# Kernel tuning notes

Hardware: AMD Instinct MI355X
Metric: run time of the kernel (lower is better)

Reference implementation:

```python
import jax, jax.numpy as jnp
import numpy as np

N = 500000
H = 256
HET = 3
AH = 128
B = 64


def setup_inputs() -> dict:
    key = jax.random.key(0)
    ks = jax.random.split(key, 6)
    x = jax.random.normal(ks[0], (N, H), dtype=jnp.float32)
    het = jax.random.uniform(ks[1], (N, HET), dtype=jnp.float32)
    batch = jnp.sort(jax.random.randint(ks[2], (N,), 0, B)).astype(jnp.int64)
    # xavier-uniform linear weights (stored already transposed: [in, out])
    def xavier(k, fan_in, fan_out):
        bound = np.sqrt(6.0 / (fan_in + fan_out))
        return jax.random.uniform(k, (fan_in, fan_out), dtype=jnp.float32,
                                  minval=-bound, maxval=bound)
    W1 = xavier(ks[3], H + HET, AH)
    b1 = jnp.zeros((AH,), dtype=jnp.float32)
    W2 = xavier(ks[4], AH, 1)
    b2 = jnp.zeros((1,), dtype=jnp.float32)
    Wv = xavier(ks[5], H, H)
    bv = jnp.zeros((H,), dtype=jnp.float32)
    return {"x": x, "het": het, "batch": batch,
            "W1": W1, "b1": b1, "W2": W2, "b2": b2, "Wv": Wv, "bv": bv}


def reference(x, het, batch, W1, b1, W2, b2, Wv, bv):
    # gate MLP: Linear -> tanh -> Linear, on [h_i ; het_i]
    gate_in = jnp.concatenate([x, het], axis=-1)              # [N, H+HET]
    raw = jnp.tanh(gate_in @ W1 + b1) @ W2 + b2               # [N, 1]
    # per-graph (segment) softmax over nodes
    seg_max = jax.ops.segment_max(raw, batch, num_segments=B)  # [B, 1]
    seg_max = jnp.where(jnp.isfinite(seg_max), seg_max, 0.0)   # empty segments
    e = jnp.exp(raw - seg_max[batch])                          # [N, 1]
    denom = jax.ops.segment_sum(e, batch, num_segments=B)      # [B, 1]
    attn = e / denom[batch]                                    # [N, 1]
    # weighted scatter-sum of projected values
    values = x @ Wv + bv                                       # [N, H]
    z = jax.ops.segment_sum(attn * values, batch, num_segments=B)  # [B, H]
    return z, attn
```

## Files before the change

kernel.cpp:

```cpp
#include <hip/hip_runtime.h>
#include <hip/hip_fp16.h>

#define H 256
#define HETD 3
#define AH 128
#define BSEG 64

typedef _Float16 half8 __attribute__((ext_vector_type(8)));
typedef __attribute__((ext_vector_type(4))) float f32x4;

__global__ void pack_w1_kernel(const float* __restrict__ W1,
                               unsigned short* __restrict__ W1p) {
    int idx = blockIdx.x * 256 + threadIdx.x;
    if (idx >= 9 * 8 * 64 * 8) return;
    int j    = idx & 7;
    int lane = (idx >> 3) & 63;
    int nt   = (idx >> 9) & 7;
    int t    = idx >> 12;
    int n = nt * 16 + (lane & 15);
    int k = t * 32 + ((lane >> 4) & 3) * 8 + j;
    float w = (k < (H + HETD)) ? W1[k * AH + n] : 0.f;
    __half hw = __float2half(w);
    W1p[idx] = __half_as_ushort(hw);
}

__device__ __forceinline__ _Float16 f2h(float f) { return (_Float16)f; }

__global__ __launch_bounds__(256) void gate_kernel(
    const float* __restrict__ x, const float* __restrict__ het,
    const int* __restrict__ batch, const unsigned short* __restrict__ W1p,
    const float* __restrict__ b1, const float* __restrict__ W2,
    const float* __restrict__ b2, float* __restrict__ p,
    float* __restrict__ d, int n_nodes)
{
    __shared__ float sW2[AH];
    __shared__ float sb1[AH];
    __shared__ float sd[BSEG];
    int tid = threadIdx.x;
    if (tid < AH) { sW2[tid] = W2[tid]; sb1[tid] = b1[tid]; }
    if (tid < BSEG) sd[tid] = 0.f;
    __syncthreads();

    int lane = tid & 63;
    int wv   = tid >> 6;
    int row  = lane & 15;
    int quad = lane >> 4;
    long long base = ((long long)blockIdx.x * 4 + wv) * 64;

    if (base < n_nodes) {
        f32x4 acc[4][8] = {};
        int nodeA[4];
#pragma unroll
        for (int m = 0; m < 4; ++m) {
            long long nd = base + m * 16 + row;
            nodeA[m] = (int)(nd < n_nodes ? nd : (long long)(n_nodes - 1));
        }
        const uint4* W1p4 = (const uint4*)W1p;

        for (int t = 0; t < 8; ++t) {
            half8 a[4];
#pragma unroll
            for (int m = 0; m < 4; ++m) {
                const float4* xr =
                    (const float4*)(x + (size_t)nodeA[m] * H + t * 32 + quad * 8);
                float4 lo = xr[0];
                float4 hi = xr[1];
                half8 av;
                av[0] = f2h(lo.x); av[1] = f2h(lo.y);
                av[2] = f2h(lo.z); av[3] = f2h(lo.w);
                av[4] = f2h(hi.x); av[5] = f2h(hi.y);
                av[6] = f2h(hi.z); av[7] = f2h(hi.w);
                a[m] = av;
            }
#pragma unroll
            for (int nt = 0; nt < 8; ++nt) {
                union { uint4 u; half8 h; } cv;
                cv.u = W1p4[(t * 8 + nt) * 64 + lane];
#pragma unroll
                for (int m = 0; m < 4; ++m)
                    acc[m][nt] = __builtin_amdgcn_mfma_f32_16x16x32_f16(
                        a[m], cv.h, acc[m][nt], 0, 0, 0);
            }
        }
        {
            half8 a[4];
#pragma unroll
            for (int m = 0; m < 4; ++m) {
                half8 av = {0, 0, 0, 0, 0, 0, 0, 0};
                if (quad == 0) {
                    const float* hr = het + (size_t)nodeA[m] * HETD;
                    av[0] = f2h(hr[0]); av[1] = f2h(hr[1]); av[2] = f2h(hr[2]);
                }
                a[m] = av;
            }
#pragma unroll
            for (int nt = 0; nt < 8; ++nt) {
                union { uint4 u; half8 h; } cv;
                cv.u = W1p4[(8 * 8 + nt) * 64 + lane];
#pragma unroll
                for (int m = 0; m < 4; ++m)
                    acc[m][nt] = __builtin_amdgcn_mfma_f32_16x16x32_f16(
                        a[m], cv.h, acc[m][nt], 0, 0, 0);
            }
        }

        float b2v = b2[0];
#pragma unroll
        for (int m = 0; m < 4; ++m) {
#pragma unroll
            for (int r = 0; r < 4; ++r) {
                float partial = 0.f;
#pragma unroll
                for (int nt = 0; nt < 8; ++nt) {
                    int n = nt * 16 + row;
                    float h = acc[m][nt][r] + sb1[n];
                    float e2 = __expf(2.f * h);
                    partial += (1.f - 2.f / (e2 + 1.f)) * sW2[n];
                }
                partial += __shfl_xor(partial, 1);
                partial += __shfl_xor(partial, 2);
                partial += __shfl_xor(partial, 4);
                partial += __shfl_xor(partial, 8);
                long long node = base + m * 16 + quad * 4 + r;
                if (row == r && node < n_nodes) {
                    float pe = __expf(partial + b2v);
                    p[node] = pe;
                    atomicAdd(&sd[batch[node]], pe);
                }
            }
        }
    }
    __syncthreads();
    if (tid < BSEG) {
        float v = sd[tid];
        if (v != 0.f) atomicAdd(&d[tid], v);
    }
}

__global__ __launch_bounds__(256) void accum_kernel(
    const float* __restrict__ x, const float* __restrict__ p,
    const int* __restrict__ batch, float* __restrict__ S, int n_nodes)
{
    const int TILE = 512;
    int tid = threadIdx.x;
    int c4 = tid & 63;
    int ng = tid >> 6;
    long long start = (long long)blockIdx.x * TILE;
    long long end = start + TILE;
    if (end > n_nodes) end = n_nodes;
    if (start >= n_nodes) return;

    float ax = 0.f, ay = 0.f, az = 0.f, aw = 0.f;
    int cur = -1;
    for (long long i = start + ng; i < end; i += 4) {
        int sg = batch[i];
        float pi = p[i];
        if (sg != cur) {
            if (cur >= 0) {
                float* Sp = S + cur * H + c4 * 4;
                atomicAdd(Sp + 0, ax); atomicAdd(Sp + 1, ay);
                atomicAdd(Sp + 2, az); atomicAdd(Sp + 3, aw);
            }
            cur = sg; ax = ay = az = aw = 0.f;
        }
        float4 xv = ((const float4*)(x + (size_t)i * H))[c4];
        ax += pi * xv.x; ay += pi * xv.y; az += pi * xv.z; aw += pi * xv.w;
    }
    if (cur >= 0) {
        float* Sp = S + cur * H + c4 * 4;
        atomicAdd(Sp + 0, ax); atomicAdd(Sp + 1, ay);
        atomicAdd(Sp + 2, az); atomicAdd(Sp + 3, aw);
    }
}

__global__ void attn_kernel(const float* __restrict__ p,
                            const int* __restrict__ batch,
                            const float* __restrict__ d,
                            float* __restrict__ attn, int n_nodes) {
    int i = blockIdx.x * 256 + threadIdx.x;
    if (i < n_nodes) attn[i] = p[i] / d[batch[i]];
}

__global__ __launch_bounds__(256) void z_kernel(
    const float* __restrict__ S, const float* __restrict__ d,
    const float* __restrict__ Wv, const float* __restrict__ bv,
    float* __restrict__ z)
{
    __shared__ float sA[H];
    int b = blockIdx.x;
    int j = threadIdx.x;
    float dv = d[b];
    float inv = (dv != 0.f) ? 1.f / dv : 0.f;
    sA[j] = S[b * H + j] * inv;
    __syncthreads();
    float sum = (dv != 0.f) ? bv[j] : 0.f;
#pragma unroll 4
    for (int h = 0; h < H; ++h)
        sum += sA[h] * Wv[h * H + j];
    z[b * H + j] = sum;
}

extern "C" void kernel_launch(void* const* d_in, const int* in_sizes, int n_in,
                              void* d_out, int out_size, void* d_ws, size_t ws_size,
                              hipStream_t stream)
{
    const float* x   = (const float*)d_in[0];
    const float* het = (const float*)d_in[1];
    const int*   bat = (const int*)d_in[2];
    const float* W1  = (const float*)d_in[3];
    const float* b1  = (const float*)d_in[4];
    const float* W2  = (const float*)d_in[5];
    const float* b2  = (const float*)d_in[6];
    const float* Wv  = (const float*)d_in[7];
    const float* bv  = (const float*)d_in[8];
    int n = in_sizes[0] / H;

    float* wsf = (float*)d_ws;
    float* d_d = wsf;
    float* d_S = wsf + BSEG;
    float* d_p = wsf + BSEG + BSEG * H;
    unsigned short* d_W1p = (unsigned short*)(wsf + BSEG + BSEG * H + n);

    hipMemsetAsync(d_d, 0, (BSEG + BSEG * H) * sizeof(float), stream);
    pack_w1_kernel<<<(9 * 8 * 64 * 8 + 255) / 256, 256, 0, stream>>>(W1, d_W1p);

    int waves = (n + 63) / 64;
    gate_kernel<<<(waves + 3) / 4, 256, 0, stream>>>(x, het, bat, d_W1p,
                                                     b1, W2, b2, d_p, d_d, n);
    accum_kernel<<<(n + 511) / 512, 256, 0, stream>>>(x, d_p, bat, d_S, n);
    attn_kernel<<<(n + 255) / 256, 256, 0, stream>>>(d_p, bat, d_d,
                                                     (float*)d_out + BSEG * H, n);
    z_kernel<<<BSEG, 256, 0, stream>>>(d_S, d_d, Wv, bv, (float*)d_out);
}
```

Before: 884.7 us.

## Fuse gate MLP and weighted accumulation into one LDS-staged kernel

Merges the gate kernel and the accumulation kernel into one kernel. Each 64-thread block stages 32 rows of x in shared memory, computes the gate scores with MFMA from LDS, then accumulates the weighted rows into per-segment sums. This removes the second full read of x from global memory. In exchange, blocks are smaller and issue many more global atomics into S. The shared memory footprint and single-wave blocks may also limit occupancy.

Result: slower. 1.113 ms (+25.8%).

```diff
diff --git a/kernel.cpp b/kernel.cpp
--- a/kernel.cpp
+++ b/kernel.cpp
@@ -5,9 +5,13 @@
 #define HETD 3
 #define AH 128
 #define BSEG 64
+#define ROWS 32
+#define LSTR 260
 
 typedef _Float16 half8 __attribute__((ext_vector_type(8)));
 typedef __attribute__((ext_vector_type(4))) float f32x4;
+
+__device__ __forceinline__ _Float16 f2h(float f) { return (_Float16)f; }
 
 __global__ void pack_w1_kernel(const float* __restrict__ W1,
                                unsigned short* __restrict__ W1p) {
@@ -24,152 +28,162 @@
     W1p[idx] = __half_as_ushort(hw);
 }
 
-__device__ __forceinline__ _Float16 f2h(float f) { return (_Float16)f; }
-
-__global__ __launch_bounds__(256) void gate_kernel(
+__global__ __launch_bounds__(64) void fused_kernel(
     const float* __restrict__ x, const float* __restrict__ het,
     const int* __restrict__ batch, const unsigned short* __restrict__ W1p,
     const float* __restrict__ b1, const float* __restrict__ W2,
     const float* __restrict__ b2, float* __restrict__ p,
-    float* __restrict__ d, int n_nodes)
+    float* __restrict__ d, float* __restrict__ S, int n_nodes)
 {
-    __shared__ float sW2[AH];
-    __shared__ float sb1[AH];
+    __shared__ float sx[ROWS * LSTR];
+    __shared__ float psh[ROWS];
+    __shared__ int   sbatch[ROWS];
     __shared__ float sd[BSEG];
-    int tid = threadIdx.x;
-    if (tid < AH) { sW2[tid] = W2[tid]; sb1[tid] = b1[tid]; }
-    if (tid < BSEG) sd[tid] = 0.f;
-    __syncthreads();
-
-    int lane = tid & 63;
-    int wv   = tid >> 6;
-    int row  = lane & 15;
-    int quad = lane >> 4;
-    long long base = ((long long)blockIdx.x * 4 + wv) * 64;
-
-    if (base < n_nodes) {
-        f32x4 acc[4][8] = {};
-        int nodeA[4];
-#pragma unroll
-        for (int m = 0; m < 4; ++m) {
-            long long nd = base + m * 16 + row;
-            nodeA[m] = (int)(nd < n_nodes ? nd : (long long)(n_nodes - 1));
-        }
-        const uint4* W1p4 = (const uint4*)W1p;
-
-        for (int t = 0; t < 8; ++t) {
-            half8 a[4];
-#pragma unroll
-            for (int m = 0; m < 4; ++m) {
-                const float4* xr =
-                    (const float4*)(x + (size_t)nodeA[m] * H + t * 32 + quad * 8);
-                float4 lo = xr[0];
-                float4 hi = xr[1];
-                half8 av;
-                av[0] = f2h(lo.x); av[1] = f2h(lo.y);
-                av[2] = f2h(lo.z); av[3] = f2h(lo.w);
-                av[4] = f2h(hi.x); av[5] = f2h(hi.y);
-                av[6] = f2h(hi.z); av[7] = f2h(hi.w);
-                a[m] = av;
-            }
+
+    const int lane = threadIdx.x;
+    const int row  = lane & 15;
+    const int quad = lane >> 4;
+    const long long base = (long long)blockIdx.x * ROWS;
+
+    sd[lane] = 0.f;
+    if (lane < ROWS) {
+        long long nd = base + lane;
+        sbatch[lane] = batch[nd < n_nodes ? nd : (long long)(n_nodes - 1)];
+    }
+
+#pragma unroll
+    for (int c = 0; c < ROWS / 16; ++c) {
+        float4 tmp[16];
+#pragma unroll
+        for (int j = 0; j < 16; ++j) {
+            long long nd = base + c * 16 + j;
+            if (nd >= n_nodes) nd = n_nodes - 1;
+            tmp[j] = ((const float4*)(x + (size_t)nd * H))[lane];
+        }
+#pragma unroll
+        for (int j = 0; j < 16; ++j)
+            *(float4*)(sx + (c * 16 + j) * LSTR + lane * 4) = tmp[j];
+    }
+
+    float w2r[8], b1r[8];
+#pragma unroll
+    for (int nt = 0; nt < 8; ++nt) {
+        w2r[nt] = W2[nt * 16 + row];
+        b1r[nt] = b1[nt * 16 + row];
+    }
+    float b2v = b2[0];
+
+    __syncthreads();
+
+    f32x4 acc[2][8] = {};
+    const uint4* W1p4 = (const uint4*)W1p;
+#pragma unroll
+    for (int t = 0; t < 8; ++t) {
+        half8 a[2];
+#pragma unroll
+        for (int m = 0; m < 2; ++m) {
+            const float4* xr =
+                (const float4*)(sx + (m * 16 + row) * LSTR + t * 32 + quad * 8);
+            float4 lo = xr[0], hi = xr[1];
+            half8 av;
+            av[0] = f2h(lo.x); av[1] = f2h(lo.y);
+            av[2] = f2h(lo.z); av[3] = f2h(lo.w);
+            av[4] = f2h(hi.x); av[5] = f2h(hi.y);
+            av[6] = f2h(hi.z); av[7] = f2h(hi.w);
+            a[m] = av;
+        }
+#pragma unroll
+        for (int nt = 0; nt < 8; ++nt) {
+            union { uint4 u; half8 h; } cv;
+            cv.u = W1p4[(t * 8 + nt) * 64 + lane];
+#pragma unroll
+            for (int m = 0; m < 2; ++m)
+                acc[m][nt] = __builtin_amdgcn_mfma_f32_16x16x32_f16(
+                    a[m], cv.h, acc[m][nt], 0, 0, 0);
+        }
+    }
+    {
+        half8 a[2];
+#pragma unroll
+        for (int m = 0; m < 2; ++m) {
+            half8 av = {0, 0, 0, 0, 0, 0, 0, 0};
+            if (quad == 0) {
+                long long nd = base + m * 16 + row;
+                if (nd >= n_nodes) nd = n_nodes - 1;
+                const float* hr = het + (size_t)nd * HETD;
+                av[0] = f2h(hr[0]); av[1] = f2h(hr[1]); av[2] = f2h(hr[2]);
+            }
+            a[m] = av;
+        }
+#pragma unroll
+        for (int nt = 0; nt < 8; ++nt) {
+            union { uint4 u; half8 h; } cv;
+            cv.u = W1p4[(8 * 8 + nt) * 64 + lane];
+#pragma unroll
+            for (int m = 0; m < 2; ++m)
+                acc[m][nt] = __builtin_amdgcn_mfma_f32_16x16x32_f16(
+                    a[m], cv.h, acc[m][nt], 0, 0, 0);
+        }
+    }
+
+#pragma unroll
+    for (int m = 0; m < 2; ++m) {
+#pragma unroll
+        for (int r = 0; r < 4; ++r) {
+            float partial = 0.f;
 #pragma unroll
             for (int nt = 0; nt < 8; ++nt) {
-                union { uint4 u; half8 h; } cv;
-                cv.u = W1p4[(t * 8 + nt) * 64 + lane];
-#pragma unroll
-                for (int m = 0; m < 4; ++m)
-                    acc[m][nt] = __builtin_amdgcn_mfma_f32_16x16x32_f16(
-                        a[m], cv.h, acc[m][nt], 0, 0, 0);
-            }
-        }
-        {
-            half8 a[4];
-#pragma unroll
-            for (int m = 0; m < 4; ++m) {
-                half8 av = {0, 0, 0, 0, 0, 0, 0, 0};
-                if (quad == 0) {
-                    const float* hr = het + (size_t)nodeA[m] * HETD;
-                    av[0] = f2h(hr[0]); av[1] = f2h(hr[1]); av[2] = f2h(hr[2]);
+                float h = acc[m][nt][r] + b1r[nt];
+                float e2 = __expf(2.f * h);
+                partial += (1.f - 2.f / (e2 + 1.f)) * w2r[nt];
+            }
+            partial += __shfl_xor(partial, 1);
+            partial += __shfl_xor(partial, 2);
+            partial += __shfl_xor(partial, 4);
+            partial += __shfl_xor(partial, 8);
+            if (row == r) {
+                int nl = m * 16 + quad * 4 + r;
+                long long node = base + nl;
+                float pe = 0.f;
+                if (node < n_nodes) {
+                    pe = __expf(partial + b2v);
+                    p[node] = pe;
+                    atomicAdd(&sd[sbatch[nl]], pe);
                 }
-                a[m] = av;
-            }
-#pragma unroll
-            for (int nt = 0; nt < 8; ++nt) {
-                union { uint4 u; half8 h; } cv;
-                cv.u = W1p4[(8 * 8 + nt) * 64 + lane];
-#pragma unroll
-                for (int m = 0; m < 4; ++m)
-                    acc[m][nt] = __builtin_amdgcn_mfma_f32_16x16x32_f16(
-                        a[m], cv.h, acc[m][nt], 0, 0, 0);
-            }
-        }
-
-        float b2v = b2[0];
-#pragma unroll
-        for (int m = 0; m < 4; ++m) {
-#pragma unroll
-            for (int r = 0; r < 4; ++r) {
-                float partial = 0.f;
-#pragma unroll
-                for (int nt = 0; nt < 8; ++nt) {
-                    int n = nt * 16 + row;
-                    float h = acc[m][nt][r] + sb1[n];
-                    float e2 = __expf(2.f * h);
-                    partial += (1.f - 2.f / (e2 + 1.f)) * sW2[n];
+                psh[nl] = pe;
+            }
+        }
+    }
+    __syncthreads();
+
+    {
+        float ax = 0.f, ay = 0.f, az = 0.f, aw = 0.f;
+        int cur = -1;
+        for (int i = 0; i < ROWS; ++i) {
+            int sg = sbatch[i];
+            float pi = psh[i];
+            if (sg != cur) {
+                if (cur >= 0) {
+                    float* Sp = S + cur * H + lane * 4;
+                    atomicAdd(Sp + 0, ax); atomicAdd(Sp + 1, ay);
+                    atomicAdd(Sp + 2, az); atomicAdd(Sp + 3, aw);
                 }
-                partial += __shfl_xor(partial, 1);
-                partial += __shfl_xor(partial, 2);
-                partial += __shfl_xor(partial, 4);
-                partial += __shfl_xor(partial, 8);
-                long long node = base + m * 16 + quad * 4 + r;
-                if (row == r && node < n_nodes) {
-                    float pe = __expf(partial + b2v);
-                    p[node] = pe;
-                    atomicAdd(&sd[batch[node]], pe);
-                }
-            }
-        }
-    }
-    __syncthreads();
-    if (tid < BSEG) {
-        float v = sd[tid];
-        if (v != 0.f) atomicAdd(&d[tid], v);
-    }
-}
-
-__global__ __launch_bounds__(256) void accum_kernel(
-    const float* __restrict__ x, const float* __restrict__ p,
-    const int* __restrict__ batch, float* __restrict__ S, int n_nodes)
-{
-    const int TILE = 512;
-    int tid = threadIdx.x;
-    int c4 = tid & 63;
-    int ng = tid >> 6;
-    long long start = (long long)blockIdx.x * TILE;
-    long long end = start + TILE;
-    if (end > n_nodes) end = n_nodes;
-    if (start >= n_nodes) return;
-
-    float ax = 0.f, ay = 0.f, az = 0.f, aw = 0.f;
-    int cur = -1;
-    for (long long i = start + ng; i < end; i += 4) {
-        int sg = batch[i];
-        float pi = p[i];
-        if (sg != cur) {
-            if (cur >= 0) {
-                float* Sp = S + cur * H + c4 * 4;
-                atomicAdd(Sp + 0, ax); atomicAdd(Sp + 1, ay);
-                atomicAdd(Sp + 2, az); atomicAdd(Sp + 3, aw);
-            }
-            cur = sg; ax = ay = az = aw = 0.f;
-        }
-        float4 xv = ((const float4*)(x + (size_t)i * H))[c4];
-        ax += pi * xv.x; ay += pi * xv.y; az += pi * xv.z; aw += pi * xv.w;
-    }
-    if (cur >= 0) {
-        float* Sp = S + cur * H + c4 * 4;
-        atomicAdd(Sp + 0, ax); atomicAdd(Sp + 1, ay);
-        atomicAdd(Sp + 2, az); atomicAdd(Sp + 3, aw);
+                cur = sg; ax = ay = az = aw = 0.f;
+            }
+            float4 xv = *(const float4*)(sx + i * LSTR + lane * 4);
+            ax += pi * xv.x; ay += pi * xv.y;
+            az += pi * xv.z; aw += pi * xv.w;
+        }
+        if (cur >= 0) {
+            float* Sp = S + cur * H + lane * 4;
+            atomicAdd(Sp + 0, ax); atomicAdd(Sp + 1, ay);
+            atomicAdd(Sp + 2, az); atomicAdd(Sp + 3, aw);
+        }
+    }
+    __syncthreads();
+    {
+        float v = sd[lane];
+        if (v != 0.f) atomicAdd(&d[lane], v);
     }
 }
 
@@ -224,10 +238,9 @@
     hipMemsetAsync(d_d, 0, (BSEG + BSEG * H) * sizeof(float), stream);
     pack_w1_kernel<<<(9 * 8 * 64 * 8 + 255) / 256, 256, 0, stream>>>(W1, d_W1p);
 
-    int waves = (n + 63) / 64;
-    gate_kernel<<<(waves + 3) / 4, 256, 0, stream>>>(x, het, bat, d_W1p,
-                                                     b1, W2, b2, d_p, d_d, n);
-    accum_kernel<<<(n + 511) / 512, 256, 0, stream>>>(x, d_p, bat, d_S, n);
+    int nblocks = (n + ROWS - 1) / ROWS;
+    fused_kernel<<<nblocks, 64, 0, stream>>>(x, het, bat, d_W1p,
+                                             b1, W2, b2, d_p, d_d, d_S, n);
     attn_kernel<<<(n + 255) / 256, 256, 0, stream>>>(d_p, bat, d_d,
                                                      (float*)d_out + BSEG * H, n);
     z_kernel<<<BSEG, 256, 0, stream>>>(d_S, d_d, Wv, bv, (float*)d_out);
```
